# Optimization experiments

Hardware: AMD Instinct MI355X
Metric: run time of the kernel (lower is better)

The kernel has to match this reference:

```python
import jax, jax.numpy as jnp
import numpy as np

N_NODES = 100000
N_EDGES = 1600000
VOCAB = 10000
HIDDEN = 64
LAYERS = 3
N_GRAPHS = 512
OUT_DIM = 1


def setup_inputs() -> dict:
    key = jax.random.key(0)
    ks = jax.random.split(key, 8)
    feats = jax.random.randint(ks[0], (N_NODES,), 0, VOCAB)
    src = jax.random.randint(ks[1], (N_EDGES,), 0, N_NODES)
    dst = jax.random.randint(ks[2], (N_EDGES,), 0, N_NODES)
    graph_ids = jnp.sort(jax.random.randint(ks[3], (N_NODES,), 0, N_GRAPHS))
    emb_table = jax.random.normal(ks[4], (VOCAB, HIDDEN), jnp.float32) * 0.02
    Ws = jax.random.normal(ks[5], (LAYERS, HIDDEN, HIDDEN), jnp.float32) * (HIDDEN ** -0.5)
    bs = jnp.zeros((LAYERS, HIDDEN), jnp.float32)
    W_reg = jax.random.normal(ks[6], (HIDDEN, OUT_DIM), jnp.float32) * (HIDDEN ** -0.5)
    return {"feats": feats, "src": src, "dst": dst, "graph_ids": graph_ids,
            "n_graphs": N_GRAPHS, "emb_table": emb_table, "Ws": Ws, "bs": bs,
            "W_reg": W_reg}


def reference(feats, src, dst, graph_ids, n_graphs, emb_table, Ws, bs, W_reg):
    N = feats.shape[0]
    ones = jnp.ones(src.shape[0], jnp.float32)
    # DGL GraphConv norm='both': src normalized by out-degree^-1/2, dst by in-degree^-1/2,
    # degrees clamped to min 1 (allow_zero_in_degree=True).
    out_deg = jnp.maximum(jax.ops.segment_sum(ones, src, num_segments=N), 1.0)
    in_deg = jnp.maximum(jax.ops.segment_sum(ones, dst, num_segments=N), 1.0)
    norm_src = (out_deg ** -0.5)[:, None]  # [N,1]
    norm_dst = (in_deg ** -0.5)[:, None]
    h = emb_table[feats]  # [N, hidden]
    for i in range(Ws.shape[0]):  # fixed small layer count
        m = h * norm_src
        agg = jax.ops.segment_sum(m[src], dst, num_segments=N)  # SpMM scatter-add
        h = agg * norm_dst @ Ws[i] + bs[i]
        # dropout p=0 -> identity
    pooled = jax.ops.segment_sum(h, graph_ids, num_segments=n_graphs)  # SumPooling
    return pooled @ W_reg
```

## Files before the change

kernel.cpp:

```cpp
#include <hip/hip_runtime.h>

#define HIDDEN 64
#define RANGE 512
#define RSHIFT 9
#define RB 256
#define NWR 1024
#define EPT 7
#define ECMAX (EPT * 256)
#define RCAP 12288
#define OUTMAX 512

__global__ __launch_bounds__(256) void pre_kernel(const float* __restrict__ emb,
                                                  const float* __restrict__ Ws,
                                                  const float* __restrict__ bs,
                                                  const float* __restrict__ Wreg,
                                                  float* __restrict__ wt,
                                                  float* __restrict__ embu, int V,
                                                  const int* __restrict__ src,
                                                  const int* __restrict__ dst,
                                                  unsigned* __restrict__ pairs,
                                                  unsigned short* __restrict__ srcb,
                                                  unsigned* __restrict__ tin,
                                                  unsigned* __restrict__ tout,
                                                  float* __restrict__ out, int out_n,
                                                  int E, int EC, int R) {
    __shared__ float u3[HIDDEN], u2[HIDDEN], u1[HIDDEN];
    __shared__ int hin[RB], hout[RB];
    __shared__ int tmp[256];
    __shared__ unsigned plds[ECMAX];
    __shared__ unsigned short slds[ECMAX];
    int t = threadIdx.x;
    int b = blockIdx.x;
    const float* W0 = Ws;
    const float* W1 = Ws + HIDDEN * HIDDEN;
    const float* W2 = Ws + 2 * HIDDEN * HIDDEN;
    if (t < HIDDEN) { float s = 0.f; for (int j = 0; j < HIDDEN; j++) s += W2[t*HIDDEN+j] * Wreg[j]; u3[t] = s; }
    __syncthreads();
    if (t < HIDDEN) { float s = 0.f; for (int j = 0; j < HIDDEN; j++) s += W1[t*HIDDEN+j] * u3[j]; u2[t] = s; }
    __syncthreads();
    if (t < HIDDEN) { float s = 0.f; for (int j = 0; j < HIDDEN; j++) s += W0[t*HIDDEN+j] * u2[j]; u1[t] = s; }
    __syncthreads();
    if (b == 0) {
        if (t < HIDDEN) {
            float c1v = bs[t] * u2[t];
            float c2v = bs[HIDDEN + t] * u3[t];
            float c3v = bs[2*HIDDEN + t] * Wreg[t];
#pragma unroll
            for (int off = 32; off > 0; off >>= 1) {
                c1v += __shfl_down(c1v, off, 64);
                c2v += __shfl_down(c2v, off, 64);
                c3v += __shfl_down(c3v, off, 64);
            }
            if (t == 0) { wt[64] = c1v; wt[65] = c2v; wt[66] = c3v; }
        }
        for (int i = t; i < out_n; i += 256) out[i] = 0.0f;
    }
    int lane = t & 63, warp = t >> 6, vs = lane >> 4, ln = lane & 15;
    int EV = (V + 15) >> 4;
    for (int task = b; task < EV; task += gridDim.x) {
        int v = task * 16 + warp * 4 + vs;
        if (v < V) {
            const float* row = emb + (size_t)v * HIDDEN;
            float acc = row[ln]*u1[ln] + row[16+ln]*u1[16+ln]
                      + row[32+ln]*u1[32+ln] + row[48+ln]*u1[48+ln];
            acc += __shfl_xor(acc, 1, 64);
            acc += __shfl_xor(acc, 2, 64);
            acc += __shfl_xor(acc, 4, 64);
            acc += __shfl_xor(acc, 8, 64);
            if (ln == 0) embu[v] = acc;
        }
    }
    int es = b * EC, ee = min(E, es + EC);
    int cntE = ee - es;
    int se[EPT], de[EPT];
#pragma unroll
    for (int k = 0; k < EPT; k++) {
        int e = es + t + (k << 8);
        bool vld = e < ee;
        se[k] = vld ? src[e] : -1;
        de[k] = vld ? dst[e] : -1;
    }
    hin[t] = 0; hout[t] = 0;
    __syncthreads();
#pragma unroll
    for (int k = 0; k < EPT; k++) {
        if (de[k] >= 0) {
            atomicAdd(&hin[de[k] >> RSHIFT], 1);
            atomicAdd(&hout[se[k] >> RSHIFT], 1);
        }
    }
    __syncthreads();
    int vin = hin[t], vout = hout[t];
    tmp[t] = vin;
    __syncthreads();
    for (int off = 1; off < 256; off <<= 1) {
        int u = (t >= off) ? tmp[t - off] : 0;
        __syncthreads();
        tmp[t] += u;
        __syncthreads();
    }
    int ein = tmp[t] - vin;
    tmp[t] = vout;
    __syncthreads();
    for (int off = 1; off < 256; off <<= 1) {
        int u = (t >= off) ? tmp[t - off] : 0;
        __syncthreads();
        tmp[t] += u;
        __syncthreads();
    }
    int eout = tmp[t] - vout;
    if (t < R) {
        tin [(size_t)t * NWR + b] = (unsigned)ein  | ((unsigned)vin  << 16);
        tout[(size_t)t * NWR + b] = (unsigned)eout | ((unsigned)vout << 16);
    }
    hin[t] = ein;
    hout[t] = eout;
    __syncthreads();
#pragma unroll
    for (int k = 0; k < EPT; k++) {
        if (de[k] >= 0) {
            int r = de[k] >> RSHIFT;
            int lr = atomicAdd(&hin[r], 1);
            if (lr < ECMAX)
                plds[lr] = ((unsigned)(de[k] - (r << RSHIFT)) << 17) | (unsigned)se[k];
            int r2 = se[k] >> RSHIFT;
            int lr2 = atomicAdd(&hout[r2], 1);
            if (lr2 < ECMAX)
                slds[lr2] = (unsigned short)(se[k] - (r2 << RSHIFT));
        }
    }
    __syncthreads();
    unsigned* pg = pairs + (size_t)b * EC;
    unsigned short* sg = srcb + (size_t)b * EC;
    for (int i = t; i < cntE; i += 256) pg[i] = plds[i];
    for (int i = t; i < cntE; i += 256) sg[i] = slds[i];
}

__global__ __launch_bounds__(256) void build_kernel(const unsigned* __restrict__ pairs,
                                                    const unsigned short* __restrict__ srcb,
                                                    const unsigned* __restrict__ tin,
                                                    const unsigned* __restrict__ tout,
                                                    const int* __restrict__ feats,
                                                    const float* __restrict__ embu,
                                                    int* __restrict__ rbeg,
                                                    int* __restrict__ rend,
                                                    int* __restrict__ col,
                                                    float* __restrict__ ndst,
                                                    float* __restrict__ nsrc,
                                                    float* __restrict__ y0,
                                                    int N, int EC) {
    __shared__ int cnt[RANGE];
    __shared__ int sc[RANGE];
    __shared__ int oh[RANGE];
    __shared__ int tmp[256];
    __shared__ unsigned pin[NWR], pout[NWR];
    int r = blockIdx.x, t = threadIdx.x;
    int n0 = r << RSHIFT;
    int nn = min(RANGE, N - n0);
    for (int i = t; i < RANGE; i += 256) { cnt[i] = 0; oh[i] = 0; }
    for (int i = t; i < NWR; i += 256) {
        pin[i]  = tin [(size_t)r * NWR + i];
        pout[i] = tout[(size_t)r * NWR + i];
    }
    __syncthreads();
    for (int b = t; b < NWR; b += 256) {
        unsigned w = pin[b];
        const unsigned* run = pairs + (size_t)b * EC + (w & 0xffff);
        int c = (int)(w >> 16);
        for (int k = 0; k < c; k++) atomicAdd(&cnt[run[k] >> 17], 1);
    }
    for (int b = t; b < NWR; b += 256) {
        unsigned w = pout[b];
        const unsigned short* run = srcb + (size_t)b * EC + (w & 0xffff);
        int c = (int)(w >> 16);
        for (int k = 0; k < c; k++) atomicAdd(&oh[run[k]], 1);
    }
    __syncthreads();
    int a0 = cnt[2 * t], a1 = cnt[2 * t + 1];
    tmp[t] = a0 + a1;
    __syncthreads();
    for (int off = 1; off < 256; off <<= 1) {
        int u = (t >= off) ? tmp[t - off] : 0;
        __syncthreads();
        tmp[t] += u;
        __syncthreads();
    }
    int c_in = tmp[255];
    int pre = (t > 0) ? tmp[t - 1] : 0;
    sc[2 * t] = pre;
    sc[2 * t + 1] = pre + a0;
    __syncthreads();
    int base = r * RCAP;
    for (int i = t; i < nn; i += 256) {
        int n = n0 + i;
        rbeg[n] = base + sc[i];
        rend[n] = base + sc[i] + cnt[i];
        ndst[n] = rsqrtf(fmaxf((float)cnt[i], 1.0f));
        float ns = rsqrtf(fmaxf((float)oh[i], 1.0f));
        nsrc[n] = ns;
        y0[n] = embu[feats[n]] * ns;
    }
    if (t < 32) col[base + c_in + t] = 0;
    __syncthreads();
    for (int b = t; b < NWR; b += 256) {
        unsigned w = pin[b];
        const unsigned* run = pairs + (size_t)b * EC + (w & 0xffff);
        int c = (int)(w >> 16);
        for (int k = 0; k < c; k++) {
            unsigned wv = run[k];
            int slot = atomicAdd(&sc[wv >> 17], 1);
            col[base + slot] = (int)(wv & 0x1ffff);
        }
    }
}

__global__ __launch_bounds__(256) void sspmm_kernel(const int* __restrict__ rbeg,
                                                    const int* __restrict__ rend,
                                                    const int* __restrict__ col,
                                                    const float* __restrict__ y,
                                                    const float* __restrict__ ndst,
                                                    const float* __restrict__ nsrc,
                                                    const float* __restrict__ wt, int cidx,
                                                    float* __restrict__ out,
                                                    int N, int NH) {
    int lane = threadIdx.x & 63;
    int warp = threadIdx.x >> 6;
    int ns_ = lane >> 4, ln = lane & 15;
    int nA = blockIdx.x * 16 + warp * 4 + ns_;
    int nB = nA + NH;
    int begA = 0, endA = 0, begB = 0, endB = 0;
    if (nA < NH) { begA = rbeg[nA]; endA = rend[nA]; }
    if (nB < N)  { begB = rbeg[nB]; endB = rend[nB]; }
    float accA = 0.0f, accB = 0.0f;
    int jA = begA + ln, jB = begB + ln;
#pragma unroll
    for (int it = 0; it < 2; it++) {
        int ja = jA + (it << 4), jb = jB + (it << 4);
        float va = y[col[ja]];
        float vb = y[col[jb]];
        accA += (ja < endA) ? va : 0.0f;
        accB += (jb < endB) ? vb : 0.0f;
    }
    for (int j = jA + 32; j < endA; j += 16) accA += y[col[j]];
    for (int j = jB + 32; j < endB; j += 16) accB += y[col[j]];
#pragma unroll
    for (int m = 1; m <= 8; m <<= 1) {
        accA += __shfl_xor(accA, m, 64);
        accB += __shfl_xor(accB, m, 64);
    }
    if (ln == 0) {
        float c = wt[cidx];
        if (nA < NH) out[nA] = (accA * ndst[nA] + c) * nsrc[nA];
        if (nB < N)  out[nB] = (accB * ndst[nB] + c) * nsrc[nB];
    }
}

__global__ __launch_bounds__(256) void sspmmf_kernel(const int* __restrict__ rbeg,
                                                     const int* __restrict__ rend,
                                                     const int* __restrict__ col,
                                                     const float* __restrict__ y,
                                                     const float* __restrict__ ndst,
                                                     const float* __restrict__ wt,
                                                     const int* __restrict__ gids,
                                                     float* __restrict__ out,
                                                     int N, int NH, int out_n) {
    __shared__ float sbin[OUTMAX];
    int t = threadIdx.x;
    for (int i = t; i < out_n; i += 256) sbin[i] = 0.0f;
    __syncthreads();
    int lane = t & 63;
    int warp = t >> 6;
    int ns_ = lane >> 4, ln = lane & 15;
    int nA = blockIdx.x * 16 + warp * 4 + ns_;
    int nB = nA + NH;
    int begA = 0, endA = 0, begB = 0, endB = 0;
    if (nA < NH) { begA = rbeg[nA]; endA = rend[nA]; }
    if (nB < N)  { begB = rbeg[nB]; endB = rend[nB]; }
    float accA = 0.0f, accB = 0.0f;
    int jA = begA + ln, jB = begB + ln;
#pragma unroll
    for (int it = 0; it < 2; it++) {
        int ja = jA + (it << 4), jb = jB + (it << 4);
        float va = y[col[ja]];
        float vb = y[col[jb]];
        accA += (ja < endA) ? va : 0.0f;
        accB += (jb < endB) ? vb : 0.0f;
    }
    for (int j = jA + 32; j < endA; j += 16) accA += y[col[j]];
    for (int j = jB + 32; j < endB; j += 16) accB += y[col[j]];
#pragma unroll
    for (int m = 1; m <= 8; m <<= 1) {
        accA += __shfl_xor(accA, m, 64);
        accB += __shfl_xor(accB, m, 64);
    }
    if (ln == 0) {
        float c = wt[66];
        if (nA < NH) atomicAdd(&sbin[gids[nA]], accA * ndst[nA] + c);
        if (nB < N)  atomicAdd(&sbin[gids[nB]], accB * ndst[nB] + c);
    }
    __syncthreads();
    for (int i = t; i < out_n; i += 256) {
        float v = sbin[i];
        if (v != 0.0f) atomicAdd(&out[i], v);
    }
}

extern "C" void kernel_launch(void* const* d_in, const int* in_sizes, int n_in,
                              void* d_out, int out_size, void* d_ws, size_t ws_size,
                              hipStream_t stream) {
    const int*   feats = (const int*)d_in[0];
    const int*   src   = (const int*)d_in[1];
    const int*   dst   = (const int*)d_in[2];
    const int*   gids  = (const int*)d_in[3];
    const float* emb   = (const float*)d_in[5];
    const float* Ws    = (const float*)d_in[6];
    const float* bs    = (const float*)d_in[7];
    const float* Wreg  = (const float*)d_in[8];
    float* out = (float*)d_out;

    int N = in_sizes[0];
    int E = in_sizes[1];
    int V = in_sizes[5] / HIDDEN;
    int R = (N + RANGE - 1) / RANGE;
    int EC = (E + NWR - 1) / NWR;
    int NH = (N + 1) / 2;
    int GS = (NH + 15) / 16;

    char* p = (char*)d_ws;
    int*   rbeg    = (int*)p;    p += (size_t)N * 4;
    int*   rend    = (int*)p;    p += (size_t)N * 4;
    float* nsrc    = (float*)p;  p += (size_t)N * 4;
    float* ndst    = (float*)p;  p += (size_t)N * 4;
    float* wt      = (float*)p;  p += 128 * 4;
    float* embu    = (float*)p;  p += (size_t)V * 4;
    float* y0      = (float*)p;  p += (size_t)N * 4;
    float* y1      = (float*)p;  p += (size_t)N * 4;
    float* y2      = (float*)p;  p += (size_t)N * 4;
    unsigned* tin  = (unsigned*)p;  p += (size_t)R * NWR * 4;
    unsigned* tout = (unsigned*)p;  p += (size_t)R * NWR * 4;
    int*   col     = (int*)p;    p += (size_t)R * RCAP * 4;
    p = (char*)(((uintptr_t)p + 255) & ~(uintptr_t)255);
    unsigned* pairs = (unsigned*)p;            p += (size_t)NWR * EC * 4;
    unsigned short* srcb = (unsigned short*)p; p += (size_t)NWR * EC * 2;

    pre_kernel<<<NWR, 256, 0, stream>>>(emb, Ws, bs, Wreg, wt, embu, V,
                                        src, dst, pairs, srcb, tin, tout,
                                        out, out_size, E, EC, R);
    build_kernel<<<R, 256, 0, stream>>>(pairs, srcb, tin, tout,
                                        feats, embu, rbeg, rend, col, ndst, nsrc, y0, N, EC);

    sspmm_kernel<<<GS, 256, 0, stream>>>(rbeg, rend, col, y0, ndst, nsrc, wt, 64, y1, N, NH);
    sspmm_kernel<<<GS, 256, 0, stream>>>(rbeg, rend, col, y1, ndst, nsrc, wt, 65, y2, N, NH);
    sspmmf_kernel<<<GS, 256, 0, stream>>>(rbeg, rend, col, y2, ndst, wt, gids, out, N, NH, out_size);
}
```

Baseline: 171.9 us.

## Halve edge-bucketing blocks and parallelize build runs across 16-lane groups

The pre kernel now uses 512 blocks instead of 1024, each handling about twice as many edges through strided loops rather than fixed per-thread register arrays. The build kernel moves to 512 threads, with one thread per node for the scan, and has 16-lane groups read each bucket run cooperatively instead of one thread walking a whole run serially. This is meant to cut the long serial per-thread loops in build and halve the per-region transpose table it has to read. In exchange, src/dst are reloaded from global memory in the second pass, and the LDS bound checks on ECMAX were removed, which relies on each block's per-region counts staying within the buffer.

```diff
diff --git a/kernel.cpp b/kernel.cpp
--- a/kernel.cpp
+++ b/kernel.cpp
@@ -4,9 +4,8 @@
 #define RANGE 512
 #define RSHIFT 9
 #define RB 256
-#define NWR 1024
-#define EPT 7
-#define ECMAX (EPT * 256)
+#define NWR 512
+#define ECMAX 3328
 #define RCAP 12288
 #define OUTMAX 512
 
@@ -70,24 +69,13 @@
             if (ln == 0) embu[v] = acc;
         }
     }
+    for (int i = t; i < RB; i += 256) { hin[i] = 0; hout[i] = 0; }
+    __syncthreads();
     int es = b * EC, ee = min(E, es + EC);
     int cntE = ee - es;
-    int se[EPT], de[EPT];
-#pragma unroll
-    for (int k = 0; k < EPT; k++) {
-        int e = es + t + (k << 8);
-        bool vld = e < ee;
-        se[k] = vld ? src[e] : -1;
-        de[k] = vld ? dst[e] : -1;
-    }
-    hin[t] = 0; hout[t] = 0;
-    __syncthreads();
-#pragma unroll
-    for (int k = 0; k < EPT; k++) {
-        if (de[k] >= 0) {
-            atomicAdd(&hin[de[k] >> RSHIFT], 1);
-            atomicAdd(&hout[se[k] >> RSHIFT], 1);
-        }
+    for (int e = es + t; e < ee; e += 256) {
+        atomicAdd(&hin[dst[e] >> RSHIFT], 1);
+        atomicAdd(&hout[src[e] >> RSHIFT], 1);
     }
     __syncthreads();
     int vin = hin[t], vout = hout[t];
@@ -116,18 +104,14 @@
     hin[t] = ein;
     hout[t] = eout;
     __syncthreads();
-#pragma unroll
-    for (int k = 0; k < EPT; k++) {
-        if (de[k] >= 0) {
-            int r = de[k] >> RSHIFT;
-            int lr = atomicAdd(&hin[r], 1);
-            if (lr < ECMAX)
-                plds[lr] = ((unsigned)(de[k] - (r << RSHIFT)) << 17) | (unsigned)se[k];
-            int r2 = se[k] >> RSHIFT;
-            int lr2 = atomicAdd(&hout[r2], 1);
-            if (lr2 < ECMAX)
-                slds[lr2] = (unsigned short)(se[k] - (r2 << RSHIFT));
-        }
+    for (int e = es + t; e < ee; e += 256) {
+        int s = src[e], d = dst[e];
+        int r = d >> RSHIFT;
+        int lr = atomicAdd(&hin[r], 1);
+        plds[lr] = ((unsigned)(d - (r << RSHIFT)) << 17) | (unsigned)s;
+        int r2 = s >> RSHIFT;
+        int lr2 = atomicAdd(&hout[r2], 1);
+        slds[lr2] = (unsigned short)(s - (r2 << RSHIFT));
     }
     __syncthreads();
     unsigned* pg = pairs + (size_t)b * EC;
@@ -136,7 +120,7 @@
     for (int i = t; i < cntE; i += 256) sg[i] = slds[i];
 }
 
-__global__ __launch_bounds__(256) void build_kernel(const unsigned* __restrict__ pairs,
+__global__ __launch_bounds__(512) void build_kernel(const unsigned* __restrict__ pairs,
                                                     const unsigned short* __restrict__ srcb,
                                                     const unsigned* __restrict__ tin,
                                                     const unsigned* __restrict__ tout,
@@ -152,61 +136,58 @@
     __shared__ int cnt[RANGE];
     __shared__ int sc[RANGE];
     __shared__ int oh[RANGE];
-    __shared__ int tmp[256];
+    __shared__ int tmp[RANGE];
     __shared__ unsigned pin[NWR], pout[NWR];
     int r = blockIdx.x, t = threadIdx.x;
     int n0 = r << RSHIFT;
     int nn = min(RANGE, N - n0);
-    for (int i = t; i < RANGE; i += 256) { cnt[i] = 0; oh[i] = 0; }
-    for (int i = t; i < NWR; i += 256) {
-        pin[i]  = tin [(size_t)r * NWR + i];
-        pout[i] = tout[(size_t)r * NWR + i];
-    }
-    __syncthreads();
-    for (int b = t; b < NWR; b += 256) {
+    cnt[t] = 0; oh[t] = 0;
+    pin[t]  = tin [(size_t)r * NWR + t];
+    pout[t] = tout[(size_t)r * NWR + t];
+    __syncthreads();
+    int g = t >> 4, ln = t & 15;
+    for (int b = g; b < NWR; b += 32) {
         unsigned w = pin[b];
         const unsigned* run = pairs + (size_t)b * EC + (w & 0xffff);
         int c = (int)(w >> 16);
-        for (int k = 0; k < c; k++) atomicAdd(&cnt[run[k] >> 17], 1);
-    }
-    for (int b = t; b < NWR; b += 256) {
+        for (int k = ln; k < c; k += 16) atomicAdd(&cnt[run[k] >> 17], 1);
+    }
+    for (int b = g; b < NWR; b += 32) {
         unsigned w = pout[b];
         const unsigned short* run = srcb + (size_t)b * EC + (w & 0xffff);
         int c = (int)(w >> 16);
-        for (int k = 0; k < c; k++) atomicAdd(&oh[run[k]], 1);
-    }
-    __syncthreads();
-    int a0 = cnt[2 * t], a1 = cnt[2 * t + 1];
-    tmp[t] = a0 + a1;
-    __syncthreads();
-    for (int off = 1; off < 256; off <<= 1) {
+        for (int k = ln; k < c; k += 16) atomicAdd(&oh[run[k]], 1);
+    }
+    __syncthreads();
+    int myc = cnt[t];
+    tmp[t] = myc;
+    __syncthreads();
+    for (int off = 1; off < 512; off <<= 1) {
         int u = (t >= off) ? tmp[t - off] : 0;
         __syncthreads();
         tmp[t] += u;
         __syncthreads();
     }
-    int c_in = tmp[255];
-    int pre = (t > 0) ? tmp[t - 1] : 0;
-    sc[2 * t] = pre;
-    sc[2 * t + 1] = pre + a0;
+    int c_in = tmp[RANGE - 1];
+    sc[t] = tmp[t] - myc;
     __syncthreads();
     int base = r * RCAP;
-    for (int i = t; i < nn; i += 256) {
-        int n = n0 + i;
-        rbeg[n] = base + sc[i];
-        rend[n] = base + sc[i] + cnt[i];
-        ndst[n] = rsqrtf(fmaxf((float)cnt[i], 1.0f));
-        float ns = rsqrtf(fmaxf((float)oh[i], 1.0f));
+    if (t < nn) {
+        int n = n0 + t;
+        rbeg[n] = base + sc[t];
+        rend[n] = base + sc[t] + myc;
+        ndst[n] = rsqrtf(fmaxf((float)myc, 1.0f));
+        float ns = rsqrtf(fmaxf((float)oh[t], 1.0f));
         nsrc[n] = ns;
         y0[n] = embu[feats[n]] * ns;
     }
     if (t < 32) col[base + c_in + t] = 0;
     __syncthreads();
-    for (int b = t; b < NWR; b += 256) {
+    for (int b = g; b < NWR; b += 32) {
         unsigned w = pin[b];
         const unsigned* run = pairs + (size_t)b * EC + (w & 0xffff);
         int c = (int)(w >> 16);
-        for (int k = 0; k < c; k++) {
+        for (int k = ln; k < c; k += 16) {
             unsigned wv = run[k];
             int slot = atomicAdd(&sc[wv >> 17], 1);
             col[base + slot] = (int)(wv & 0x1ffff);
@@ -346,7 +327,7 @@
     pre_kernel<<<NWR, 256, 0, stream>>>(emb, Ws, bs, Wreg, wt, embu, V,
                                         src, dst, pairs, srcb, tin, tout,
                                         out, out_size, E, EC, R);
-    build_kernel<<<R, 256, 0, stream>>>(pairs, srcb, tin, tout,
+    build_kernel<<<R, 512, 0, stream>>>(pairs, srcb, tin, tout,
                                         feats, embu, rbeg, rend, col, ndst, nsrc, y0, N, EC);
 
     sspmm_kernel<<<GS, 256, 0, stream>>>(rbeg, rend, col, y0, ndst, nsrc, wt, 64, y1, N, NH);
```

After: 172.8 us. No clear change (+0.5%).

## Halve edge-binning block count and loop over edges from global memory

Applied to the files above, without the earlier changes.

Cuts the number of edge-partition blocks from 1024 to 512, so each block bins about twice as many edges (up to 3328) and the per-bin transpose tables the build stage reads shrink by half. The register-held fixed EPT edge arrays are replaced by strided loops that read src/dst from global memory twice, once for the histogram and once for the scatter. This lowers the per-range metadata and prefix work downstream, at the cost of less parallelism in the pre-kernel, a second pass over the edge arrays, and removal of the ECMAX bounds checks on the LDS writes.

```diff
diff --git a/kernel.cpp b/kernel.cpp
--- a/kernel.cpp
+++ b/kernel.cpp
@@ -4,9 +4,8 @@
 #define RANGE 512
 #define RSHIFT 9
 #define RB 256
-#define NWR 1024
-#define EPT 7
-#define ECMAX (EPT * 256)
+#define NWR 512
+#define ECMAX 3328
 #define RCAP 12288
 #define OUTMAX 512
 
@@ -70,24 +69,13 @@
             if (ln == 0) embu[v] = acc;
         }
     }
+    for (int i = t; i < RB; i += 256) { hin[i] = 0; hout[i] = 0; }
+    __syncthreads();
     int es = b * EC, ee = min(E, es + EC);
     int cntE = ee - es;
-    int se[EPT], de[EPT];
-#pragma unroll
-    for (int k = 0; k < EPT; k++) {
-        int e = es + t + (k << 8);
-        bool vld = e < ee;
-        se[k] = vld ? src[e] : -1;
-        de[k] = vld ? dst[e] : -1;
-    }
-    hin[t] = 0; hout[t] = 0;
-    __syncthreads();
-#pragma unroll
-    for (int k = 0; k < EPT; k++) {
-        if (de[k] >= 0) {
-            atomicAdd(&hin[de[k] >> RSHIFT], 1);
-            atomicAdd(&hout[se[k] >> RSHIFT], 1);
-        }
+    for (int e = es + t; e < ee; e += 256) {
+        atomicAdd(&hin[dst[e] >> RSHIFT], 1);
+        atomicAdd(&hout[src[e] >> RSHIFT], 1);
     }
     __syncthreads();
     int vin = hin[t], vout = hout[t];
@@ -116,18 +104,14 @@
     hin[t] = ein;
     hout[t] = eout;
     __syncthreads();
-#pragma unroll
-    for (int k = 0; k < EPT; k++) {
-        if (de[k] >= 0) {
-            int r = de[k] >> RSHIFT;
-            int lr = atomicAdd(&hin[r], 1);
-            if (lr < ECMAX)
-                plds[lr] = ((unsigned)(de[k] - (r << RSHIFT)) << 17) | (unsigned)se[k];
-            int r2 = se[k] >> RSHIFT;
-            int lr2 = atomicAdd(&hout[r2], 1);
-            if (lr2 < ECMAX)
-                slds[lr2] = (unsigned short)(se[k] - (r2 << RSHIFT));
-        }
+    for (int e = es + t; e < ee; e += 256) {
+        int s = src[e], d = dst[e];
+        int r = d >> RSHIFT;
+        int lr = atomicAdd(&hin[r], 1);
+        plds[lr] = ((unsigned)(d - (r << RSHIFT)) << 17) | (unsigned)s;
+        int r2 = s >> RSHIFT;
+        int lr2 = atomicAdd(&hout[r2], 1);
+        slds[lr2] = (unsigned short)(s - (r2 << RSHIFT));
     }
     __syncthreads();
     unsigned* pg = pairs + (size_t)b * EC;
```

Result: faster. 166.0 us (-3.4%).
